# Kernel optimization log

Hardware: AMD Instinct MI355X
Metric: run time of the kernel (lower is better)

Reference implementation:

```python
import jax, jax.numpy as jnp
import numpy as np


def _interp1d(xq, yq, xnew):
    """torchinterp1d semantics: linear interp with end-slope extrapolation.
    xq: (Q,) nondecreasing knots, yq: (Q,) values, xnew: any shape."""
    ind = jnp.clip(jnp.searchsorted(xq, xnew), 1, xq.shape[0] - 1)
    x0 = xq[ind - 1]
    x1 = xq[ind]
    y0 = yq[ind - 1]
    y1 = yq[ind]
    return y0 + (y1 - y0) / (x1 - x0) * (xnew - x0)


def setup_inputs() -> dict:
    key = jax.random.key(0)
    k1, k2 = jax.random.split(key)
    x = jax.random.normal(k1, (64, 512, 2048), dtype=jnp.float32)  # (N, C, L)
    target_quantiles = jax.random.uniform(k2, (256,), dtype=jnp.float32)  # sorted inside reference, as in the module
    return {"x": x, "target_quantiles": target_quantiles}


def reference(x, target_quantiles):
    # BatchOT forward (training=True, batchwise_matching=True, smoothing=None).
    C = x.shape[1]
    xt = jnp.moveaxis(x, 1, -1)        # (N, ..., C)
    flat = xt.reshape(-1, C)           # (M, C)
    Q = target_quantiles.shape[0]
    qs = jnp.linspace(0.0, 1.0, Q, dtype=x.dtype)      # buffer `quantiles`
    # per-feature batch quantiles, torch.quantile default 'linear' interpolation
    sq = jnp.quantile(flat, qs, axis=0)                # (Q, C)
    sq = jnp.sort(sq, axis=0)
    tq = jnp.sort(target_quantiles)
    # 1) map data through inverse source quantile fn, per feature: (M, C) -> [0,1]
    u = jax.vmap(_interp1d, in_axes=(1, None, 1), out_axes=1)(sq, qs, flat)
    u = jnp.clip(u, 0.0, 1.0)
    # 2) map quantile levels through the target quantile function (shared knots)
    y = _interp1d(qs, tq, u)           # (M, C)
    y = y.reshape(xt.shape)
    return jnp.moveaxis(y, -1, 1)      # (N, C, ...)
```

## Files before the change

### kernel.cpp

```cpp
#include <hip/hip_runtime.h>
#include <stdint.h>

#define N_   64
#define C_   512
#define L_   2048
#define M_   131072
#define Q_   256
#define NR_  512
#define NL_  (C_ * L_)
#define CAP_ 7168

__device__ __forceinline__ uint32_t f2u(float f) {
    uint32_t u = __float_as_uint(f);
    return u ^ ((uint32_t)((int32_t)u >> 31) | 0x80000000u);
}
__device__ __forceinline__ float u2f(uint32_t u) {
    uint32_t v = (u & 0x80000000u) ? (u ^ 0x80000000u) : ~u;
    return __uint_as_float(v);
}
__device__ __forceinline__ uint32_t h0pad(uint32_t b) { return b + (b >> 5); }

__global__ void sort_tq_kernel(const float* __restrict__ tq_in, float* __restrict__ tq_out) {
    __shared__ float s[Q_];
    int t = threadIdx.x;
    s[t] = tq_in[t];
    __syncthreads();
    for (int k = 2; k <= Q_; k <<= 1) {
        for (int j = k >> 1; j > 0; j >>= 1) {
            int ixj = t ^ j;
            if (ixj > t) {
                float a = s[t], b = s[ixj];
                bool up = ((t & k) == 0);
                if ((a > b) == up) { s[t] = b; s[ixj] = a; }
            }
            __syncthreads();
        }
    }
    tq_out[t] = s[t];
}

__device__ __forceinline__ uint32_t waveScan(uint32_t v, int lane) {
    #pragma unroll
    for (int off = 1; off < 64; off <<= 1) {
        uint32_t t = __shfl_up(v, off, 64);
        if (lane >= off) v += t;
    }
    return v;
}
__device__ __forceinline__ uint32_t blockScan(uint32_t v, uint32_t* wsum, int tid) {
    const int lane = tid & 63, wid = tid >> 6;
    uint32_t s = waveScan(v, lane);
    if (lane == 63) wsum[wid] = s;
    __syncthreads();
    if (wid == 0) {
        uint32_t w = (lane < 16) ? wsum[lane] : 0u;
        w = waveScan(w, lane);
        if (lane < 16) wsum[lane] = w;
    }
    __syncthreads();
    uint32_t r = s + ((wid > 0) ? wsum[wid - 1] : 0u);
    __syncthreads();
    return r;
}

__device__ __forceinline__ uint32_t dedupe512(uint32_t* keys, uint32_t* wsum, uint32_t* gout,
                                              uint32_t mykey, int tid, uint32_t* headOut) {
    if (tid < NR_) keys[tid] = mykey;
    __syncthreads();
    uint32_t h = 0;
    if (tid < NR_) h = (tid == 0) ? 1u : ((keys[tid] != keys[tid - 1]) ? 1u : 0u);
    uint32_t incl = blockScan(h, wsum, tid);
    if (tid == NR_ - 1) *gout = incl;
    *headOut = h;
    return incl - 1u;
}

__device__ __forceinline__ uint32_t rank_walk8(const uint32_t* rows, uint32_t slot, uint32_t& lrnk) {
    uint32_t acc = 0, dig = 0;
    bool found = false;
    const uint32_t* r = rows + slot * 17u;
    #pragma unroll
    for (int w = 0; w < 16; ++w) {
        uint32_t word = r[w];
        #pragma unroll
        for (int b = 0; b < 4; ++b) {
            uint32_t cnt = (word >> (8 * b)) & 255u;
            if (!found) {
                if (acc + cnt > lrnk) { dig = 4u * w + b; found = true; } else acc += cnt;
            }
        }
    }
    lrnk -= acc;
    return dig;
}

#define SM_KEYS 16896
#define SM_WSUM 17408
#define SM_M1   17424
#define SM_BS1  18448
#define SM_CNT2 18960
#define SM_BASE 19472
#define SM_GC   19984
#define SM_WORDS 19988

__global__ __launch_bounds__(1024, 8) void qsel_kernel(const float* __restrict__ x,
                                                       const float* __restrict__ tqs,
                                                       float* __restrict__ out) {
    __shared__ uint32_t smem[SM_WORDS];
    uint32_t* hist0   = smem;
    uint32_t* selBit  = smem;
    uint32_t* selBase = smem + 512;
    uint32_t* rows    = smem + 1024;
    uint32_t* candK   = smem + 1024;
    uint32_t* candS   = smem + 8192;
    float*    ssq     = (float*)(smem + 1024);
    float4*   kt      = (float4*)(smem + 1280);
    uint32_t* tblw    = smem + 2304;
    uint16_t* tbl16   = (uint16_t*)(smem + 2304);
    uint32_t* keys    = smem + SM_KEYS;
    uint32_t* wsum    = smem + SM_WSUM;
    uint2*    m1      = (uint2*)(smem + SM_M1);
    uint32_t* bs1     = smem + SM_BS1;
    uint32_t* cnt2    = smem + SM_CNT2;
    uint32_t* base    = smem + SM_BASE;
    uint32_t* gc      = smem + SM_GC;

    const int c = blockIdx.x, tid = threadIdx.x;
    const float* xc = x + (size_t)c * L_;
    float*       oc = out + (size_t)c * L_;
    const int l4 = (tid & 511) << 2;
    const int n0 = tid >> 9;

    uint32_t lrnk = 0;
    if (tid < NR_) {
        int k = tid >> 1;
        float pos = ((float)k / 255.0f) * 131071.0f;
        int lo = (int)floorf(pos);
        if (lo > M_ - 1) lo = M_ - 1;
        if (lo < 0) lo = 0;
        int r = (tid & 1) ? ((lo + 1 > M_ - 1) ? M_ - 1 : lo + 1) : lo;
        lrnk = (uint32_t)r;
    }

    for (int i = tid; i < 16896; i += 1024) hist0[i] = 0u;
    if (tid < 4) gc[tid] = 0u;
    __syncthreads();
    for (int nn = n0; nn < N_; nn += 8) {
        float4 a = *reinterpret_cast<const float4*>(xc + (size_t)nn       * NL_ + l4);
        float4 b = *reinterpret_cast<const float4*>(xc + (size_t)(nn + 2) * NL_ + l4);
        float4 d = *reinterpret_cast<const float4*>(xc + (size_t)(nn + 4) * NL_ + l4);
        float4 e = *reinterpret_cast<const float4*>(xc + (size_t)(nn + 6) * NL_ + l4);
        float vv[16] = {a.x,a.y,a.z,a.w, b.x,b.y,b.z,b.w, d.x,d.y,d.z,d.w, e.x,e.y,e.z,e.w};
        #pragma unroll
        for (int q = 0; q < 16; ++q)
            atomicAdd(&hist0[h0pad(f2u(vv[q]) >> 18)], 1u);
    }
    __syncthreads();

    {
        uint32_t bb = (uint32_t)tid * 16u; bb += (bb >> 5);
        uint32_t acc = 0;
        #pragma unroll
        for (int i = 0; i < 16; ++i) { acc += hist0[bb + i]; hist0[bb + i] = acc; }
        uint32_t excl = blockScan(acc, wsum, tid) - acc;
        #pragma unroll
        for (int i = 0; i < 16; ++i) hist0[bb + i] += excl;
    }
    __syncthreads();

    uint32_t mykey = 0;
    if (tid < NR_) {
        uint32_t d = 0;
        #pragma unroll
        for (uint32_t s = 8192; s > 0; s >>= 1)
            if (d + s <= 16384u && hist0[h0pad(d + s - 1u)] <= lrnk) d += s;
        uint32_t below = d ? hist0[h0pad(d - 1u)] : 0u;
        mykey = d;
        lrnk -= below;
    }
    __syncthreads();

    uint32_t head;
    uint32_t slot = dedupe512(keys, wsum, gc + 0, mykey, tid, &head);
    __syncthreads();

    if (tid < 512) { selBit[tid] = 0u; selBase[tid] = 0u; m1[tid] = make_uint2(0u, 0u); }
    for (int i = 1024 + tid; i < 9728; i += 1024) smem[i] = 0u;
    __syncthreads();
    if (tid < NR_ && head) atomicOr(&selBit[mykey >> 5], 1u << (mykey & 31u));
    __syncthreads();
    {
        uint32_t pc = (tid < 512) ? __popc(selBit[tid]) : 0u;
        uint32_t incl = blockScan(pc, wsum, tid);
        if (tid < 512) selBase[tid] = incl - pc;
    }
    __syncthreads();

    for (int nn = n0; nn < N_; nn += 8) {
        float4 a = *reinterpret_cast<const float4*>(xc + (size_t)nn       * NL_ + l4);
        float4 b = *reinterpret_cast<const float4*>(xc + (size_t)(nn + 2) * NL_ + l4);
        float4 d = *reinterpret_cast<const float4*>(xc + (size_t)(nn + 4) * NL_ + l4);
        float4 e = *reinterpret_cast<const float4*>(xc + (size_t)(nn + 6) * NL_ + l4);
        float vv[16] = {a.x,a.y,a.z,a.w, b.x,b.y,b.z,b.w, d.x,d.y,d.z,d.w, e.x,e.y,e.z,e.w};
        #pragma unroll
        for (int q = 0; q < 16; ++q) {
            uint32_t key = f2u(vv[q]);
            uint32_t bin = key >> 18;
            uint32_t w = selBit[bin >> 5];
            uint32_t bt = bin & 31u;
            if ((w >> bt) & 1u) {
                uint32_t slt = selBase[bin >> 5] + __popc(w & ((1u << bt) - 1u));
                uint32_t dd = (key >> 12) & 63u;
                atomicAdd(&rows[slt * 17u + (dd >> 2)], 1u << ((dd & 3u) << 3));
            }
        }
    }
    __syncthreads();

    uint32_t dig = 0;
    if (tid < NR_) { dig = rank_walk8(rows, slot, lrnk); mykey = (mykey << 6) | dig; }
    __syncthreads();
    uint32_t head1;
    uint32_t g1 = dedupe512(keys, wsum, gc + 1, mykey, tid, &head1);
    if (tid < NR_ && head1)
        atomicOr(&((uint32_t*)m1)[2u * slot + (dig >> 5)], 1u << (dig & 31u));
    if (tid == 0) gc[2] = 0u;
    if (tid < 512) cnt2[tid] = 0u;
    __syncthreads();
    {
        uint32_t S = gc[0];
        uint32_t pc = (tid < (int)S) ? (__popc(m1[tid].x) + __popc(m1[tid].y)) : 0u;
        uint32_t incl = blockScan(pc, wsum, tid);
        if (tid < 512) bs1[tid] = incl - pc;
    }
    __syncthreads();

    for (int nn = n0; nn < N_; nn += 8) {
        float4 a = *reinterpret_cast<const float4*>(xc + (size_t)nn       * NL_ + l4);
        float4 b = *reinterpret_cast<const float4*>(xc + (size_t)(nn + 2) * NL_ + l4);
        float4 d = *reinterpret_cast<const float4*>(xc + (size_t)(nn + 4) * NL_ + l4);
        float4 e = *reinterpret_cast<const float4*>(xc + (size_t)(nn + 6) * NL_ + l4);
        float vv[16] = {a.x,a.y,a.z,a.w, b.x,b.y,b.z,b.w, d.x,d.y,d.z,d.w, e.x,e.y,e.z,e.w};
        #pragma unroll
        for (int q = 0; q < 16; ++q) {
            uint32_t key = f2u(vv[q]);
            uint32_t bin = key >> 18;
            uint32_t w = selBit[bin >> 5];
            uint32_t bt = bin & 31u;
            if (!((w >> bt) & 1u)) continue;
            uint32_t slt = selBase[bin >> 5] + __popc(w & ((1u << bt) - 1u));
            uint2 mm = m1[slt];
            uint32_t dd = (key >> 12) & 63u;
            uint32_t mw = (dd < 32u) ? mm.x : mm.y;
            uint32_t db = dd & 31u;
            if (!((mw >> db) & 1u)) continue;
            uint32_t g = bs1[slt] + ((dd < 32u) ? __popc(mm.x & ((1u << db) - 1u))
                                                : __popc(mm.x) + __popc(mm.y & ((1u << db) - 1u)));
            uint32_t pos = atomicAdd(&gc[2], 1u);
            if (pos < CAP_) candK[pos] = key;
            atomicAdd(&cnt2[g], 1u);
        }
    }
    __syncthreads();

    uint32_t G1 = gc[1];
    uint32_t total = gc[2]; if (total > CAP_) total = CAP_;
    {
        uint32_t cv = (tid < (int)G1) ? cnt2[tid] : 0u;
        uint32_t incl = blockScan(cv, wsum, tid);
        if (tid < 512) { base[tid] = incl - cv; cnt2[tid] = 0u; }
    }
    __syncthreads();
    for (int i = tid; i < (int)total; i += 1024) {
        uint32_t key = candK[i];
        uint32_t bin = key >> 18;
        uint32_t w = selBit[bin >> 5];
        uint32_t bt = bin & 31u;
        uint32_t slt = selBase[bin >> 5] + __popc(w & ((1u << bt) - 1u));
        uint2 mm = m1[slt];
        uint32_t dd = (key >> 12) & 63u;
        uint32_t db = dd & 31u;
        uint32_t g = bs1[slt] + ((dd < 32u) ? __popc(mm.x & ((1u << db) - 1u))
                                            : __popc(mm.x) + __popc(mm.y & ((1u << db) - 1u)));
        uint32_t j = base[g] + atomicAdd(&cnt2[g], 1u);
        if (j < CAP_) candS[j] = key;
    }
    __syncthreads();

    uint32_t finalKey = 0;
    if (tid < NR_) {
        uint32_t b = base[g1];
        uint32_t n = ((g1 + 1u < G1) ? base[g1 + 1u] : total) - b;
        for (uint32_t i = 0; i < n; ++i) {
            uint32_t ki = candS[b + i];
            uint32_t clt = 0, ceq = 0;
            for (uint32_t j = 0; j < n; ++j) {
                uint32_t kj = candS[b + j];
                clt += (kj < ki) ? 1u : 0u;
                ceq += (kj == ki) ? 1u : 0u;
            }
            if (clt <= lrnk && lrnk < clt + ceq) { finalKey = ki; break; }
        }
    }
    __syncthreads();
    if (tid < NR_) keys[tid] = finalKey;
    __syncthreads();

    if (tid < Q_) {
        float pos = ((float)tid / 255.0f) * 131071.0f;
        float fr  = pos - floorf(pos);
        float vlo = u2f(keys[2 * tid]);
        float vhi = u2f(keys[2 * tid + 1]);
        ssq[tid] = vlo + fr * (vhi - vlo);
    }
    for (int i = tid; i < 8192; i += 1024) tblw[i] = 0u;
    __syncthreads();

    if (tid < Q_) {
        if (tid >= 1) {
            float x0 = ssq[tid - 1], x1 = ssq[tid];
            float y0 = tqs[tid - 1], y1 = tqs[tid];
            float dx = x1 - x0;
            kt[tid] = make_float4(x0, 1.0f / dx, y0, y1 - y0);
        }
        uint32_t kb = f2u(ssq[tid]) >> 18;
        atomicAdd(&tblw[kb >> 1], 1u << ((kb & 1u) << 4));
    }
    __syncthreads();

    {
        uint32_t bw = (uint32_t)tid * 8u;
        uint32_t w[8];
        #pragma unroll
        for (int i = 0; i < 8; ++i) w[i] = tblw[bw + i];
        uint32_t sum = 0;
        #pragma unroll
        for (int i = 0; i < 8; ++i) sum += (w[i] & 0xFFFFu) + (w[i] >> 16);
        uint32_t run = blockScan(sum, wsum, tid) - sum;
        #pragma unroll
        for (int i = 0; i < 8; ++i) {
            uint32_t c0 = w[i] & 0xFFFFu, c1 = w[i] >> 16;
            uint32_t e0 = run | (c0 ? 0x8000u : 0u); run += c0;
            uint32_t e1 = run | (c1 ? 0x8000u : 0u); run += c1;
            tblw[bw + i] = e0 | (e1 << 16);
        }
    }
    __syncthreads();

    for (int nn = n0; nn < N_; nn += 4) {
        const float4 a = *reinterpret_cast<const float4*>(xc + (size_t)nn       * NL_ + l4);
        const float4 b = *reinterpret_cast<const float4*>(xc + (size_t)(nn + 2) * NL_ + l4);
        float4 oa, ob;
        #pragma unroll
        for (int h = 0; h < 8; ++h) {
            float v = (h == 0) ? a.x : (h == 1) ? a.y : (h == 2) ? a.z : (h == 3) ? a.w
                    : (h == 4) ? b.x : (h == 5) ? b.y : (h == 6) ? b.z : b.w;
            uint32_t e = tbl16[f2u(v) >> 18];
            uint32_t t = e & 0x7FFFu;
            if (e & 0x8000u) {
                while (t < 256u && ssq[t] < v) ++t;
            }
            uint32_t ind = (t < 1u) ? 1u : ((t > 255u) ? 255u : t);
            float4 k = kt[ind];
            float r = (v - k.x) * k.y;
            r = fminf(fmaxf(r, 0.0f), 1.0f);
            float y = k.z + k.w * r;
            if      (h == 0) oa.x = y; else if (h == 1) oa.y = y;
            else if (h == 2) oa.z = y; else if (h == 3) oa.w = y;
            else if (h == 4) ob.x = y; else if (h == 5) ob.y = y;
            else if (h == 6) ob.z = y; else               ob.w = y;
        }
        *reinterpret_cast<float4*>(oc + (size_t)nn       * NL_ + l4) = oa;
        *reinterpret_cast<float4*>(oc + (size_t)(nn + 2) * NL_ + l4) = ob;
    }
}

extern "C" void kernel_launch(void* const* d_in, const int* in_sizes, int n_in,
                              void* d_out, int out_size, void* d_ws, size_t ws_size,
                              hipStream_t stream) {
    const float* x     = (const float*)d_in[0];
    const float* tq_in = (const float*)d_in[1];
    float* out = (float*)d_out;

    float* tqs = (float*)d_ws;

    sort_tq_kernel<<<1, Q_, 0, stream>>>(tq_in, tqs);
    qsel_kernel<<<C_, 1024, 0, stream>>>(x, tqs, out);
}
```

Measured before the change: 283.5 us.

## Replace bitmap bin lookup with direct slot table and scatter candidates directly

Replaces the selected-bin bitmap plus popcount prefix with a 16-bit bin-to-slot lookup table filled with sentinel values, cutting several barriers and a block scan. Per-group candidate counts are now read directly from the second-level histogram, so group bases are computed before the second pass. Candidates are scattered straight into sorted-group positions, which removes the intermediate candidate buffer, the extra scan and the redistribution loop. The cost is a larger lookup-table initialisation and reliance on the 8-bit packed histogram counts being exact for group sizes.

```diff
diff --git a/kernel.cpp b/kernel.cpp
--- a/kernel.cpp
+++ b/kernel.cpp
@@ -107,23 +107,21 @@
                                                        const float* __restrict__ tqs,
                                                        float* __restrict__ out) {
     __shared__ uint32_t smem[SM_WORDS];
-    uint32_t* hist0   = smem;
-    uint32_t* selBit  = smem;
-    uint32_t* selBase = smem + 512;
-    uint32_t* rows    = smem + 1024;
-    uint32_t* candK   = smem + 1024;
-    uint32_t* candS   = smem + 8192;
-    float*    ssq     = (float*)(smem + 1024);
-    float4*   kt      = (float4*)(smem + 1280);
-    uint32_t* tblw    = smem + 2304;
-    uint16_t* tbl16   = (uint16_t*)(smem + 2304);
-    uint32_t* keys    = smem + SM_KEYS;
-    uint32_t* wsum    = smem + SM_WSUM;
-    uint2*    m1      = (uint2*)(smem + SM_M1);
-    uint32_t* bs1     = smem + SM_BS1;
-    uint32_t* cnt2    = smem + SM_CNT2;
-    uint32_t* base    = smem + SM_BASE;
-    uint32_t* gc      = smem + SM_GC;
+    uint32_t* hist0    = smem;
+    uint16_t* binslot  = (uint16_t*)smem;
+    uint32_t* rows     = smem + 8192;
+    uint32_t* candS    = smem + 8192;
+    float*    ssq      = (float*)(smem + 1024);
+    float4*   kt       = (float4*)(smem + 1280);
+    uint32_t* tblw     = smem + 2304;
+    uint16_t* tbl16    = (uint16_t*)(smem + 2304);
+    uint32_t* keys     = smem + SM_KEYS;
+    uint32_t* wsum     = smem + SM_WSUM;
+    uint2*    m1       = (uint2*)(smem + SM_M1);
+    uint32_t* bs1      = smem + SM_BS1;
+    uint32_t* cnt2     = smem + SM_CNT2;
+    uint32_t* base     = smem + SM_BASE;
+    uint32_t* gc       = smem + SM_GC;
 
     const int c = blockIdx.x, tid = threadIdx.x;
     const float* xc = x + (size_t)c * L_;
@@ -182,18 +180,11 @@
 
     uint32_t head;
     uint32_t slot = dedupe512(keys, wsum, gc + 0, mykey, tid, &head);
-    __syncthreads();
-
-    if (tid < 512) { selBit[tid] = 0u; selBase[tid] = 0u; m1[tid] = make_uint2(0u, 0u); }
-    for (int i = 1024 + tid; i < 9728; i += 1024) smem[i] = 0u;
-    __syncthreads();
-    if (tid < NR_ && head) atomicOr(&selBit[mykey >> 5], 1u << (mykey & 31u));
-    __syncthreads();
-    {
-        uint32_t pc = (tid < 512) ? __popc(selBit[tid]) : 0u;
-        uint32_t incl = blockScan(pc, wsum, tid);
-        if (tid < 512) selBase[tid] = incl - pc;
-    }
+
+    for (int i = tid; i < 16896; i += 1024) smem[i] = (i < 8192) ? 0xFFFFFFFFu : 0u;
+    if (tid < 512) m1[tid] = make_uint2(0u, 0u);
+    __syncthreads();
+    if (tid < NR_ && head) binslot[mykey] = (uint16_t)slot;
     __syncthreads();
 
     for (int nn = n0; nn < N_; nn += 8) {
@@ -205,26 +196,25 @@
         #pragma unroll
         for (int q = 0; q < 16; ++q) {
             uint32_t key = f2u(vv[q]);
-            uint32_t bin = key >> 18;
-            uint32_t w = selBit[bin >> 5];
-            uint32_t bt = bin & 31u;
-            if ((w >> bt) & 1u) {
-                uint32_t slt = selBase[bin >> 5] + __popc(w & ((1u << bt) - 1u));
+            uint32_t s = binslot[key >> 18];
+            if (s != 0xFFFFu) {
                 uint32_t dd = (key >> 12) & 63u;
-                atomicAdd(&rows[slt * 17u + (dd >> 2)], 1u << ((dd & 3u) << 3));
-            }
-        }
-    }
-    __syncthreads();
-
-    uint32_t dig = 0;
-    if (tid < NR_) { dig = rank_walk8(rows, slot, lrnk); mykey = (mykey << 6) | dig; }
-    __syncthreads();
+                atomicAdd(&rows[s * 17u + (dd >> 2)], 1u << ((dd & 3u) << 3));
+            }
+        }
+    }
+    __syncthreads();
+
+    uint32_t dig = 0, cntg = 0;
+    if (tid < NR_) {
+        dig = rank_walk8(rows, slot, lrnk);
+        mykey = (mykey << 6) | dig;
+        cntg = (rows[slot * 17u + (dig >> 2)] >> ((dig & 3u) << 3)) & 255u;
+    }
     uint32_t head1;
     uint32_t g1 = dedupe512(keys, wsum, gc + 1, mykey, tid, &head1);
     if (tid < NR_ && head1)
         atomicOr(&((uint32_t*)m1)[2u * slot + (dig >> 5)], 1u << (dig & 31u));
-    if (tid == 0) gc[2] = 0u;
     if (tid < 512) cnt2[tid] = 0u;
     __syncthreads();
     {
@@ -232,6 +222,12 @@
         uint32_t pc = (tid < (int)S) ? (__popc(m1[tid].x) + __popc(m1[tid].y)) : 0u;
         uint32_t incl = blockScan(pc, wsum, tid);
         if (tid < 512) bs1[tid] = incl - pc;
+    }
+    {
+        uint32_t cv = (tid < NR_ && head1) ? cntg : 0u;
+        uint32_t incl = blockScan(cv, wsum, tid);
+        if (tid < NR_ && head1) base[g1] = incl - cv;
+        if (tid == NR_ - 1) gc[2] = incl;
     }
     __syncthreads();
 
@@ -244,49 +240,23 @@
         #pragma unroll
         for (int q = 0; q < 16; ++q) {
             uint32_t key = f2u(vv[q]);
-            uint32_t bin = key >> 18;
-            uint32_t w = selBit[bin >> 5];
-            uint32_t bt = bin & 31u;
-            if (!((w >> bt) & 1u)) continue;
-            uint32_t slt = selBase[bin >> 5] + __popc(w & ((1u << bt) - 1u));
-            uint2 mm = m1[slt];
+            uint32_t s = binslot[key >> 18];
+            if (s == 0xFFFFu) continue;
+            uint2 mm = m1[s];
             uint32_t dd = (key >> 12) & 63u;
             uint32_t mw = (dd < 32u) ? mm.x : mm.y;
             uint32_t db = dd & 31u;
             if (!((mw >> db) & 1u)) continue;
-            uint32_t g = bs1[slt] + ((dd < 32u) ? __popc(mm.x & ((1u << db) - 1u))
-                                                : __popc(mm.x) + __popc(mm.y & ((1u << db) - 1u)));
-            uint32_t pos = atomicAdd(&gc[2], 1u);
-            if (pos < CAP_) candK[pos] = key;
-            atomicAdd(&cnt2[g], 1u);
+            uint32_t g = bs1[s] + ((dd < 32u) ? __popc(mm.x & ((1u << db) - 1u))
+                                              : __popc(mm.x) + __popc(mm.y & ((1u << db) - 1u)));
+            uint32_t j = base[g] + atomicAdd(&cnt2[g], 1u);
+            if (j < CAP_) candS[j] = key;
         }
     }
     __syncthreads();
 
     uint32_t G1 = gc[1];
     uint32_t total = gc[2]; if (total > CAP_) total = CAP_;
-    {
-        uint32_t cv = (tid < (int)G1) ? cnt2[tid] : 0u;
-        uint32_t incl = blockScan(cv, wsum, tid);
-        if (tid < 512) { base[tid] = incl - cv; cnt2[tid] = 0u; }
-    }
-    __syncthreads();
-    for (int i = tid; i < (int)total; i += 1024) {
-        uint32_t key = candK[i];
-        uint32_t bin = key >> 18;
-        uint32_t w = selBit[bin >> 5];
-        uint32_t bt = bin & 31u;
-        uint32_t slt = selBase[bin >> 5] + __popc(w & ((1u << bt) - 1u));
-        uint2 mm = m1[slt];
-        uint32_t dd = (key >> 12) & 63u;
-        uint32_t db = dd & 31u;
-        uint32_t g = bs1[slt] + ((dd < 32u) ? __popc(mm.x & ((1u << db) - 1u))
-                                            : __popc(mm.x) + __popc(mm.y & ((1u << db) - 1u)));
-        uint32_t j = base[g] + atomicAdd(&cnt2[g], 1u);
-        if (j < CAP_) candS[j] = key;
-    }
-    __syncthreads();
-
     uint32_t finalKey = 0;
     if (tid < NR_) {
         uint32_t b = base[g1];
```

After: 271.8 us, median of 2. -4.1%, faster.
